# Kernel optimization log

Measured on AMD Instinct MI355X. Metric: run time of the kernel, lower is better.

## Reference

```python
import jax, jax.numpy as jnp
import numpy as np

N = 50000     # nodes
E = 800000    # edges (before self-loops)
DIN = 128     # input feature dim
DH = 16       # per-head hidden dim (layer 1)
H = 8         # heads (layer 1)
DOUT = 64     # output classes (layer 2, heads=1)


def setup_inputs() -> dict:
    key = jax.random.key(0)
    ks = jax.random.split(key, 10)
    def rn(k, shape, scale=0.1):
        return jax.random.normal(k, shape, dtype=jnp.float32) * scale
    x = jax.random.normal(ks[0], (N, DIN), dtype=jnp.float32)
    edge_index = jax.random.randint(ks[1], (2, E), 0, N, dtype=jnp.int64)
    return {
        "x": x,
        "edge_index": edge_index,
        "W1": rn(ks[2], (DIN, H * DH)),
        "a_src1": rn(ks[3], (H, DH)),
        "a_dst1": rn(ks[4], (H, DH)),
        "b1": jnp.zeros((H * DH,), jnp.float32),
        "W2": rn(ks[5], (H * DH, DOUT)),
        "a_src2": rn(ks[6], (1, DOUT)),
        "a_dst2": rn(ks[7], (1, DOUT)),
        "b2": jnp.zeros((DOUT,), jnp.float32),
    }


def gat_conv(x, src, dst, W, a_src, a_dst, b, heads, out_dim):
    """PyG-style GATConv: edge attention + segment softmax over dst + scatter-add."""
    n = x.shape[0]
    h = (x @ W).reshape(n, heads, out_dim)                 # [N, H, D]
    alpha_src = jnp.sum(h * a_src, axis=-1)                # [N, H]
    alpha_dst = jnp.sum(h * a_dst, axis=-1)                # [N, H]
    e = jax.nn.leaky_relu(alpha_src[src] + alpha_dst[dst], 0.2)  # [Etot, H]
    # numerically-stable segment softmax grouped by destination node
    m = jax.ops.segment_max(e, dst, num_segments=n)        # [N, H]
    ex = jnp.exp(e - m[dst])
    s = jax.ops.segment_sum(ex, dst, num_segments=n)       # [N, H]
    alpha = ex / (s[dst] + 1e-16)                          # [Etot, H]
    msg = h[src] * alpha[..., None]                        # [Etot, H, D]
    out = jax.ops.segment_sum(msg, dst, num_segments=n)    # [N, H, D]
    return out.reshape(n, heads * out_dim) + b


def reference(x, W1, a_src1, a_dst1, b1, W2, a_src2, a_dst2, b2, edge_index):
    # eval mode: F.dropout(p=0.6, training=False) is identity
    loop = jnp.arange(N, dtype=edge_index.dtype)
    src = jnp.concatenate([edge_index[0], loop])  # add_self_loops=True (PyG default)
    dst = jnp.concatenate([edge_index[1], loop])
    h = gat_conv(x, src, dst, W1, a_src1, a_dst1, b1, H, DH)
    h = jax.nn.elu(h)
    h = gat_conv(h, src, dst, W2, a_src2, a_dst2, b2, 1, DOUT)
    return (h, jax.nn.log_softmax(h, axis=1))
```

## Files before the change

kernel.cpp:

```cpp
#include <hip/hip_runtime.h>

#define NN 50000
#define EE 800000
#define ET (EE + NN)
#define NCH ((NN + 255) / 256)
#define DEGB ((ET + 255) / 256)
#define WPB ((128 * 128 + 128 * 64 + 255) / 256)
#define GEMB ((NN + 63) / 64)

typedef unsigned short ushort_t;
using bf16x8 = __attribute__((ext_vector_type(8))) short;
using f32x4  = __attribute__((ext_vector_type(4))) float;

__device__ __forceinline__ float bf2f(ushort_t u) {
    return __uint_as_float(((unsigned int)u) << 16);
}
__device__ __forceinline__ ushort_t f2bf(float f) {
    unsigned int u = __float_as_uint(f);
    u += 0x7fffu + ((u >> 16) & 1u);
    return (ushort_t)(u >> 16);
}
__device__ __forceinline__ float lrelu(float e) {
    return fmaxf(e, 0.f) + 0.2f * fminf(e, 0.f);
}
__device__ __forceinline__ float ldf(const void* p, int i, bool f32) {
    return f32 ? ((const float*)p)[i] : bf2f(((const ushort_t*)p)[i]);
}

__device__ __forceinline__ bool sniff_f32(const unsigned int* __restrict__ xw) {
    int lane = threadIdx.x & 63;
    float v = __uint_as_float(xw[lane]);
    float a = fabsf(v);
    bool ok = (a > 1e-6f && a < 1e6f) || v == 0.f;
    unsigned long long m = __ballot(ok);
    return __popcll(m) >= 48;
}
__device__ __forceinline__ bool sniff_i64(const int* __restrict__ eiw) {
    int lane = threadIdx.x & 63;
    unsigned long long m = __ballot(eiw[2 * lane + 1] != 0);
    return __popcll(m) <= 4;
}

__device__ __forceinline__ void edge_sd(const int* ei, int i, bool i64, int& s, int& d) {
    if (i < EE) {
        if (i64) { s = ei[2 * i]; d = ei[2 * (EE + i)]; }
        else     { s = ei[i];     d = ei[EE + i]; }
    } else {
        s = d = i - EE;
    }
}
__device__ __forceinline__ int edge_d(const int* ei, int i, bool i64) {
    if (i < EE) return i64 ? ei[2 * (EE + i)] : ei[EE + i];
    return i - EE;
}

__global__ __launch_bounds__(256) void prep_kernel(const int* __restrict__ ei, int* __restrict__ deg8,
                                                   const unsigned int* __restrict__ xw,
                                                   const void* W1v, const void* W2v,
                                                   ushort_t* __restrict__ Wt1, ushort_t* __restrict__ Wt2) {
    int b = blockIdx.x;
    if (b < DEGB) {
        bool i64 = sniff_i64(ei);
        int i = b * 256 + threadIdx.x;
        if (i >= ET) return;
        int g = b & 7;
        int d = edge_d(ei, i, i64);
        atomicAdd(&deg8[(size_t)g * NN + d], 1);
    } else {
        bool f32 = sniff_f32(xw);
        int i = (b - DEGB) * 256 + threadIdx.x;
        if (i < 128 * 128) {
            int k = i >> 7, nc = i & 127;
            ushort_t v = f32 ? f2bf(((const float*)W1v)[i]) : ((const ushort_t*)W1v)[i];
            Wt1[nc * 128 + k] = v;
        }
        int j = i - 128 * 128;
        if (j >= 0 && j < 128 * 64) {
            int k = j >> 6, nc = j & 63;
            ushort_t v = f32 ? f2bf(((const float*)W2v)[j]) : ((const ushort_t*)W2v)[j];
            Wt2[nc * 128 + k] = v;
        }
    }
}

#define FLG_A (1ull << 62)
#define FLG_P (2ull << 62)

__device__ void scan_body(int b, int* __restrict__ deg8, int* __restrict__ rowptr,
                          unsigned long long* __restrict__ state) {
    __shared__ int wsum[4];
    __shared__ int bpref;
    int t = threadIdx.x;
    int node = b * 256 + t;
    int lane = t & 63, wid = t >> 6;
    int dv[8];
    int v = 0;
    if (node < NN) {
        #pragma unroll
        for (int g = 0; g < 8; ++g) {
            dv[g] = deg8[(size_t)g * NN + node];
            v += dv[g];
        }
    }
    int x = v;
    #pragma unroll
    for (int off = 1; off < 64; off <<= 1) {
        int y = __shfl_up(x, off);
        if (lane >= off) x += y;
    }
    if (lane == 63) wsum[wid] = x;
    __syncthreads();
    if (t < 4) {
        int s = wsum[t];
        #pragma unroll
        for (int off = 1; off < 4; off <<= 1) {
            int y = __shfl_up(s, off);
            if (t >= off) s += y;
        }
        wsum[t] = s;
    }
    __syncthreads();
    int total = wsum[3];
    if (t == 0) {
        int prefix = 0;
        if (b == 0) {
            atomicExch(&state[0], FLG_P | (unsigned long long)(unsigned)total);
        } else {
            atomicExch(&state[b], FLG_A | (unsigned long long)(unsigned)total);
            int j = b - 1;
            while (true) {
                unsigned long long sv = atomicAdd(&state[j], 0ull);
                unsigned long long f = sv >> 62;
                if (f == 0) { __builtin_amdgcn_s_sleep(2); continue; }
                prefix += (int)(unsigned)(sv & 0xffffffffull);
                if (f == 2) break;
                --j;
            }
            atomicExch(&state[b], FLG_P | (unsigned long long)(unsigned)(prefix + total));
        }
        bpref = prefix;
    }
    __syncthreads();
    int excl = x - v + ((wid > 0) ? wsum[wid - 1] : 0);
    if (node < NN) {
        int run = bpref + excl;
        rowptr[node] = run;
        #pragma unroll
        for (int g = 0; g < 8; ++g) {
            deg8[(size_t)g * NN + node] = run;
            run += dv[g];
        }
    }
    if (b == NCH - 1 && t == 255) rowptr[NN] = bpref + total;
}

template <bool AEXT, int NCOL, int NH>
__device__ __forceinline__ void mgemm_body(int bid, const void* Av, const ushort_t* __restrict__ Wt,
                                           const void* a_src, const void* a_dst,
                                           ushort_t* __restrict__ outb, float* __restrict__ asrc,
                                           float* __restrict__ adst, int n, bool f32) {
    constexpr int K = 128;
    constexpr int NCT = NCOL / 16;
    bool af32 = AEXT && f32;
    int t = threadIdx.x;
    int lane = t & 63, wid = t >> 6;
    int m = lane & 15, quad = lane >> 4;
    int rbase = bid * 64 + wid * 16;
    int row = rbase + m;
    bool rok = row < n;

    bf16x8 af[4];
    if (rok) {
        if (!af32) {
            const ushort_t* ap = (const ushort_t*)Av + (size_t)row * K + quad * 8;
            #pragma unroll
            for (int kk = 0; kk < 4; ++kk) af[kk] = *(const bf16x8*)(ap + kk * 32);
        } else {
            const float* ap = (const float*)Av + (size_t)row * K + quad * 8;
            #pragma unroll
            for (int kk = 0; kk < 4; ++kk) {
                float4 q0 = *(const float4*)(ap + kk * 32);
                float4 q1 = *(const float4*)(ap + kk * 32 + 4);
                bf16x8 v;
                v[0] = (short)f2bf(q0.x); v[1] = (short)f2bf(q0.y);
                v[2] = (short)f2bf(q0.z); v[3] = (short)f2bf(q0.w);
                v[4] = (short)f2bf(q1.x); v[5] = (short)f2bf(q1.y);
                v[6] = (short)f2bf(q1.z); v[7] = (short)f2bf(q1.w);
                af[kk] = v;
            }
        }
    } else {
        #pragma unroll
        for (int kk = 0; kk < 4; ++kk) af[kk] = (bf16x8){0, 0, 0, 0, 0, 0, 0, 0};
    }

    f32x4 acc[NCT];
    #pragma unroll
    for (int c = 0; c < NCT; ++c) acc[c] = (f32x4){0.f, 0.f, 0.f, 0.f};

    const ushort_t* wp = Wt + (size_t)m * K + quad * 8;
    #pragma unroll
    for (int c = 0; c < NCT; ++c) {
        const ushort_t* wc = wp + (size_t)c * 16 * K;
        #pragma unroll
        for (int kk = 0; kk < 4; ++kk) {
            bf16x8 bf = *(const bf16x8*)(wc + kk * 32);
            acc[c] = __builtin_amdgcn_mfma_f32_16x16x32_bf16(af[kk], bf, acc[c], 0, 0, 0);
        }
    }

    int orow0 = rbase + quad * 4;
    #pragma unroll
    for (int c = 0; c < NCT; ++c) {
        #pragma unroll
        for (int r = 0; r < 4; ++r) {
            int orow = orow0 + r;
            if (orow < n) outb[(size_t)orow * NCOL + c * 16 + m] = f2bf(acc[c][r]);
        }
    }

    if (NH == 8) {
        #pragma unroll
        for (int c = 0; c < NCT; ++c) {
            float as = ldf(a_src, c * 16 + m, f32);
            float ad = ldf(a_dst, c * 16 + m, f32);
            float ps[4], pd[4];
            #pragma unroll
            for (int r = 0; r < 4; ++r) { ps[r] = acc[c][r] * as; pd[r] = acc[c][r] * ad; }
            #pragma unroll
            for (int stp = 1; stp < 16; stp <<= 1) {
                #pragma unroll
                for (int r = 0; r < 4; ++r) {
                    ps[r] += __shfl_xor(ps[r], stp);
                    pd[r] += __shfl_xor(pd[r], stp);
                }
            }
            if (m == 0) {
                #pragma unroll
                for (int r = 0; r < 4; ++r) {
                    int orow = orow0 + r;
                    if (orow < n) {
                        asrc[(size_t)orow * 8 + c] = ps[r];
                        adst[(size_t)orow * 8 + c] = pd[r];
                    }
                }
            }
        }
    } else {
        float ps[4] = {0.f, 0.f, 0.f, 0.f}, pd[4] = {0.f, 0.f, 0.f, 0.f};
        #pragma unroll
        for (int c = 0; c < NCT; ++c) {
            float as = ldf(a_src, c * 16 + m, f32);
            float ad = ldf(a_dst, c * 16 + m, f32);
            #pragma unroll
            for (int r = 0; r < 4; ++r) {
                ps[r] = fmaf(acc[c][r], as, ps[r]);
                pd[r] = fmaf(acc[c][r], ad, pd[r]);
            }
        }
        #pragma unroll
        for (int stp = 1; stp < 16; stp <<= 1) {
            #pragma unroll
            for (int r = 0; r < 4; ++r) {
                ps[r] += __shfl_xor(ps[r], stp);
                pd[r] += __shfl_xor(pd[r], stp);
            }
        }
        if (m == 0) {
            #pragma unroll
            for (int r = 0; r < 4; ++r) {
                int orow = orow0 + r;
                if (orow < n) { asrc[orow] = ps[r]; adst[orow] = pd[r]; }
            }
        }
    }
}

__global__ __launch_bounds__(256) void scan_mgemm1_kernel(int* __restrict__ deg8, int* __restrict__ rowptr,
                                                          unsigned long long* __restrict__ state,
                                                          const void* xv, const ushort_t* __restrict__ Wt1,
                                                          const void* as1, const void* ad1,
                                                          ushort_t* __restrict__ h1b,
                                                          float* __restrict__ asrc1, float* __restrict__ adst1) {
    if (blockIdx.x < NCH) {
        scan_body(blockIdx.x, deg8, rowptr, state);
        return;
    }
    bool f32 = sniff_f32((const unsigned int*)xv);
    mgemm_body<true, 128, 8>(blockIdx.x - NCH, xv, Wt1, as1, ad1, h1b, asrc1, adst1, NN, f32);
}

__global__ __launch_bounds__(256) void mgemm2_kernel(const void* Av, const ushort_t* __restrict__ Wt,
                                                     const void* a_src, const void* a_dst,
                                                     ushort_t* __restrict__ outb, float* __restrict__ asrc,
                                                     float* __restrict__ adst, const unsigned int* __restrict__ xw) {
    bool f32 = sniff_f32(xw);
    mgemm_body<false, 64, 1>(blockIdx.x, Av, Wt, a_src, a_dst, outb, asrc, adst, NN, f32);
}

__global__ __launch_bounds__(256) void fill_kernel(const int* __restrict__ ei, int* __restrict__ deg8,
                                                   int* __restrict__ col) {
    bool i64 = sniff_i64(ei);
    int i = blockIdx.x * 256 + threadIdx.x;
    if (i >= ET) return;
    int g = blockIdx.x & 7;
    int s, d;
    edge_sd(ei, i, i64, s, d);
    int pos = atomicAdd(&deg8[(size_t)g * NN + d], 1);
    col[pos] = s;
}

__global__ __launch_bounds__(256) void agg1_kernel(const unsigned int* __restrict__ xw,
                                                   const int* __restrict__ rowptr, const int* __restrict__ col,
                                                   const ushort_t* __restrict__ h1b,
                                                   const float* __restrict__ asrc, const float* __restrict__ adst,
                                                   const void* b1, ushort_t* __restrict__ hmidb) {
    __shared__ float wle[4][8 * 72];
    __shared__ int loff[4][64];
    bool f32 = sniff_f32(xw);
    int lane = threadIdx.x & 63, wid = threadIdx.x >> 6;
    int d = blockIdx.x * 4 + wid;
    if (d >= NN) return;
    int start = rowptr[d], end = rowptr[d + 1];
    int hB = lane >> 3;
    const float4* dp = (const float4*)(adst + (size_t)d * 8);
    float4 ad0 = dp[0], ad1 = dp[1];
    const char* hb = (const char*)h1b + lane * 4;
    float acc0 = 0.f, acc1 = 0.f, ssum = 0.f;
    for (int chunk = start; chunk < end; chunk += 64) {
        int cnt = min(64, end - chunk);
        int c = (chunk + lane < end) ? col[chunk + lane] : 0;
        loff[wid][lane] = c << 8;
        if (lane < cnt) {
            const float4* ap = (const float4*)(asrc + (size_t)c * 8);
            float4 s0 = ap[0], s1 = ap[1];
            wle[wid][0 * 72 + lane] = __expf(lrelu(s0.x + ad0.x));
            wle[wid][1 * 72 + lane] = __expf(lrelu(s0.y + ad0.y));
            wle[wid][2 * 72 + lane] = __expf(lrelu(s0.z + ad0.z));
            wle[wid][3 * 72 + lane] = __expf(lrelu(s0.w + ad0.w));
            wle[wid][4 * 72 + lane] = __expf(lrelu(s1.x + ad1.x));
            wle[wid][5 * 72 + lane] = __expf(lrelu(s1.y + ad1.y));
            wle[wid][6 * 72 + lane] = __expf(lrelu(s1.z + ad1.z));
            wle[wid][7 * 72 + lane] = __expf(lrelu(s1.w + ad1.w));
        }
        #pragma unroll 4
        for (int j = 0; j < cnt; ++j) {
            int off = loff[wid][j];
            float ex = wle[wid][hB * 72 + j];
            unsigned int hv = *(const unsigned int*)(hb + off);
            ssum += ex;
            acc0 = fmaf(ex, __uint_as_float(hv << 16), acc0);
            acc1 = fmaf(ex, __uint_as_float(hv & 0xffff0000u), acc1);
        }
    }
    float inv = 1.f / (ssum + 1e-16f);
    float o0 = fmaf(acc0, inv, ldf(b1, lane * 2, f32));
    float o1 = fmaf(acc1, inv, ldf(b1, lane * 2 + 1, f32));
    o0 = (o0 > 0.f) ? o0 : (__expf(o0) - 1.f);
    o1 = (o1 > 0.f) ? o1 : (__expf(o1) - 1.f);
    unsigned int pk = ((unsigned int)f2bf(o1) << 16) | (unsigned int)f2bf(o0);
    *(unsigned int*)(hmidb + (size_t)d * 128 + lane * 2) = pk;
}

__global__ __launch_bounds__(256) void agg2_kernel(const unsigned int* __restrict__ xw,
                                                   const int* __restrict__ rowptr, const int* __restrict__ col,
                                                   const ushort_t* __restrict__ h2b,
                                                   const float* __restrict__ asrc, const float* __restrict__ adst,
                                                   const void* b2, float* __restrict__ out) {
    __shared__ float wle[4][64];
    __shared__ int loff[4][64];
    bool f32 = sniff_f32(xw);
    int lane = threadIdx.x & 63, wid = threadIdx.x >> 6;
    int d = blockIdx.x * 4 + wid;
    if (d >= NN) return;
    int start = rowptr[d], end = rowptr[d + 1];
    float ad = adst[d];
    const char* hb = (const char*)h2b + lane * 2;
    float acc = 0.f, ssum = 0.f;
    for (int chunk = start; chunk < end; chunk += 64) {
        int cnt = min(64, end - chunk);
        int c = (chunk + lane < end) ? col[chunk + lane] : 0;
        loff[wid][lane] = c << 7;
        if (lane < cnt) wle[wid][lane] = __expf(lrelu(asrc[c] + ad));
        #pragma unroll 4
        for (int j = 0; j < cnt; ++j) {
            int off = loff[wid][j];
            float ex = wle[wid][j];
            float hv = bf2f(*(const ushort_t*)(hb + off));
            ssum += ex;
            acc = fmaf(ex, hv, acc);
        }
    }
    float o = acc / (ssum + 1e-16f) + ldf(b2, lane, f32);
    float mm = o;
    #pragma unroll
    for (int off = 1; off < 64; off <<= 1) mm = fmaxf(mm, __shfl_xor(mm, off));
    float texp = __expf(o - mm);
    float ts = texp;
    #pragma unroll
    for (int off = 1; off < 64; off <<= 1) ts += __shfl_xor(ts, off);
    float ls = o - mm - __logf(ts);
    out[(size_t)d * 64 + lane] = o;
    out[(size_t)NN * 64 + (size_t)d * 64 + lane] = ls;
}

extern "C" void kernel_launch(void* const* d_in, const int* in_sizes, int n_in,
                              void* d_out, int out_size, void* d_ws, size_t ws_size,
                              hipStream_t stream) {
    const void* x   = d_in[0];
    const int*  ei  = (const int*)d_in[1];
    const void* W1  = d_in[2];
    const void* as1 = d_in[3];
    const void* ad1 = d_in[4];
    const void* b1  = d_in[5];
    const void* W2  = d_in[6];
    const void* as2 = d_in[7];
    const void* ad2 = d_in[8];
    const void* b2  = d_in[9];
    float* out = (float*)d_out;

    char* w = (char*)d_ws;
    auto alloc = [&](size_t bytes) {
        void* p = (void*)w;
        w += (bytes + 255) & ~(size_t)255;
        return p;
    };
    int* deg8     = (int*)alloc((size_t)8 * NN * 4 + 4096);
    unsigned long long* state = (unsigned long long*)((char*)deg8 + (size_t)8 * NN * 4);
    int* rowptr   = (int*)alloc((size_t)(NN + 1) * 4);
    int* colx     = (int*)alloc((size_t)ET * 4);
    ushort_t* Wt1 = (ushort_t*)alloc((size_t)128 * 128 * 2);
    ushort_t* Wt2 = (ushort_t*)alloc((size_t)64 * 128 * 2);
    ushort_t* h1b = (ushort_t*)alloc((size_t)NN * 128 * 2);
    float* asrc1  = (float*)alloc((size_t)NN * 8 * 4);
    float* adst1  = (float*)alloc((size_t)NN * 8 * 4);
    ushort_t* hmidb = (ushort_t*)alloc((size_t)NN * 128 * 2);
    ushort_t* h2b = (ushort_t*)alloc((size_t)NN * 64 * 2);
    float* asrc2  = (float*)alloc((size_t)NN * 4);
    float* adst2  = (float*)alloc((size_t)NN * 4);

    hipMemsetAsync(deg8, 0, (size_t)8 * NN * 4 + (size_t)NCH * 8, stream);

    prep_kernel<<<DEGB + WPB, 256, 0, stream>>>(ei, deg8, (const unsigned int*)x, W1, W2, Wt1, Wt2);
    scan_mgemm1_kernel<<<NCH + GEMB, 256, 0, stream>>>(deg8, rowptr, state, x, Wt1, as1, ad1,
                                                       h1b, asrc1, adst1);
    fill_kernel<<<DEGB, 256, 0, stream>>>(ei, deg8, colx);
    agg1_kernel<<<(NN + 3) / 4, 256, 0, stream>>>((const unsigned int*)x, rowptr, colx, h1b,
                                                  asrc1, adst1, b1, hmidb);
    mgemm2_kernel<<<GEMB, 256, 0, stream>>>((const void*)hmidb, Wt2, as2, ad2, h2b, asrc2, adst2,
                                            (const unsigned int*)x);
    agg2_kernel<<<(NN + 3) / 4, 256, 0, stream>>>((const unsigned int*)x, rowptr, colx, h2b,
                                                  asrc2, adst2, b2, out);
}
```

Baseline: 291.6 us.

## Record edge ranks in degree count, atomic-free CSR fill fused with GEMM1

Result: faster. 253.4 us (-13.1%).

```diff
diff --git a/kernel.cpp b/kernel.cpp
--- a/kernel.cpp
+++ b/kernel.cpp
@@ -55,6 +55,7 @@
 }
 
 __global__ __launch_bounds__(256) void prep_kernel(const int* __restrict__ ei, int* __restrict__ deg8,
+                                                   int* __restrict__ rank,
                                                    const unsigned int* __restrict__ xw,
                                                    const void* W1v, const void* W2v,
                                                    ushort_t* __restrict__ Wt1, ushort_t* __restrict__ Wt2) {
@@ -65,7 +66,7 @@
         if (i >= ET) return;
         int g = b & 7;
         int d = edge_d(ei, i, i64);
-        atomicAdd(&deg8[(size_t)g * NN + d], 1);
+        rank[i] = atomicAdd(&deg8[(size_t)g * NN + d], 1);
     } else {
         bool f32 = sniff_f32(xw);
         int i = (b - DEGB) * 256 + threadIdx.x;
@@ -84,12 +85,12 @@
 }
 
 #define FLG_A (1ull << 62)
-#define FLG_P (2ull << 62)
-
-__device__ void scan_body(int b, int* __restrict__ deg8, int* __restrict__ rowptr,
-                          unsigned long long* __restrict__ state) {
+
+__global__ __launch_bounds__(256) void scan_kernel(int* __restrict__ deg8, int* __restrict__ rowptr,
+                                                   unsigned long long* __restrict__ state) {
     __shared__ int wsum[4];
     __shared__ int bpref;
+    int b = blockIdx.x;
     int t = threadIdx.x;
     int node = b * 256 + t;
     int lane = t & 63, wid = t >> 6;
@@ -121,24 +122,21 @@
     }
     __syncthreads();
     int total = wsum[3];
-    if (t == 0) {
-        int prefix = 0;
-        if (b == 0) {
-            atomicExch(&state[0], FLG_P | (unsigned long long)(unsigned)total);
-        } else {
-            atomicExch(&state[b], FLG_A | (unsigned long long)(unsigned)total);
-            int j = b - 1;
-            while (true) {
-                unsigned long long sv = atomicAdd(&state[j], 0ull);
-                unsigned long long f = sv >> 62;
-                if (f == 0) { __builtin_amdgcn_s_sleep(2); continue; }
-                prefix += (int)(unsigned)(sv & 0xffffffffull);
-                if (f == 2) break;
-                --j;
-            }
-            atomicExch(&state[b], FLG_P | (unsigned long long)(unsigned)(prefix + total));
-        }
-        bpref = prefix;
+    if (t == 0) atomicExch(&state[b], FLG_A | (unsigned long long)(unsigned)total);
+    if (t < 64) {
+        int p = 0;
+        #pragma unroll
+        for (int w = 0; w < (NCH + 63) / 64; ++w) {
+            int j = w * 64 + t;
+            unsigned long long sv = 0;
+            if (j < b) {
+                do { sv = atomicAdd(&state[j], 0ull); __builtin_amdgcn_s_sleep(1); } while (!(sv >> 62));
+            }
+            p += (int)(unsigned)(sv & 0xffffffffull);
+        }
+        #pragma unroll
+        for (int off = 1; off < 64; off <<= 1) p += __shfl_xor(p, off);
+        if (t == 0) bpref = p;
     }
     __syncthreads();
     int excl = x - v + ((wid > 0) ? wsum[wid - 1] : 0);
@@ -151,7 +149,7 @@
             run += dv[g];
         }
     }
-    if (b == NCH - 1 && t == 255) rowptr[NN] = bpref + total;
+    if (b == NCH - 1 && t == 0) rowptr[NN] = bpref + total;
 }
 
 template <bool AEXT, int NCOL, int NH>
@@ -276,18 +274,26 @@
     }
 }
 
-__global__ __launch_bounds__(256) void scan_mgemm1_kernel(int* __restrict__ deg8, int* __restrict__ rowptr,
-                                                          unsigned long long* __restrict__ state,
-                                                          const void* xv, const ushort_t* __restrict__ Wt1,
-                                                          const void* as1, const void* ad1,
-                                                          ushort_t* __restrict__ h1b,
-                                                          float* __restrict__ asrc1, float* __restrict__ adst1) {
-    if (blockIdx.x < NCH) {
-        scan_body(blockIdx.x, deg8, rowptr, state);
+__global__ __launch_bounds__(256) void gemm1_fill_kernel(const void* xv, const ushort_t* __restrict__ Wt1,
+                                                         const void* as1, const void* ad1,
+                                                         ushort_t* __restrict__ h1b,
+                                                         float* __restrict__ asrc1, float* __restrict__ adst1,
+                                                         const int* __restrict__ ei,
+                                                         const int* __restrict__ deg8off,
+                                                         const int* __restrict__ rank, int* __restrict__ col) {
+    if (blockIdx.x < GEMB) {
+        bool f32 = sniff_f32((const unsigned int*)xv);
+        mgemm_body<true, 128, 8>(blockIdx.x, xv, Wt1, as1, ad1, h1b, asrc1, adst1, NN, f32);
         return;
     }
-    bool f32 = sniff_f32((const unsigned int*)xv);
-    mgemm_body<true, 128, 8>(blockIdx.x - NCH, xv, Wt1, as1, ad1, h1b, asrc1, adst1, NN, f32);
+    int bb = blockIdx.x - GEMB;
+    bool i64 = sniff_i64(ei);
+    int i = bb * 256 + threadIdx.x;
+    if (i >= ET) return;
+    int g = bb & 7;
+    int s, d;
+    edge_sd(ei, i, i64, s, d);
+    col[deg8off[(size_t)g * NN + d] + rank[i]] = s;
 }
 
 __global__ __launch_bounds__(256) void mgemm2_kernel(const void* Av, const ushort_t* __restrict__ Wt,
@@ -296,18 +302,6 @@
                                                      float* __restrict__ adst, const unsigned int* __restrict__ xw) {
     bool f32 = sniff_f32(xw);
     mgemm_body<false, 64, 1>(blockIdx.x, Av, Wt, a_src, a_dst, outb, asrc, adst, NN, f32);
-}
-
-__global__ __launch_bounds__(256) void fill_kernel(const int* __restrict__ ei, int* __restrict__ deg8,
-                                                   int* __restrict__ col) {
-    bool i64 = sniff_i64(ei);
-    int i = blockIdx.x * 256 + threadIdx.x;
-    if (i >= ET) return;
-    int g = blockIdx.x & 7;
-    int s, d;
-    edge_sd(ei, i, i64, s, d);
-    int pos = atomicAdd(&deg8[(size_t)g * NN + d], 1);
-    col[pos] = s;
 }
 
 __global__ __launch_bounds__(256) void agg1_kernel(const unsigned int* __restrict__ xw,
@@ -343,7 +337,7 @@
             wle[wid][6 * 72 + lane] = __expf(lrelu(s1.z + ad1.z));
             wle[wid][7 * 72 + lane] = __expf(lrelu(s1.w + ad1.w));
         }
-        #pragma unroll 4
+        #pragma unroll 8
         for (int j = 0; j < cnt; ++j) {
             int off = loff[wid][j];
             float ex = wle[wid][hB * 72 + j];
@@ -382,7 +376,7 @@
         int c = (chunk + lane < end) ? col[chunk + lane] : 0;
         loff[wid][lane] = c << 7;
         if (lane < cnt) wle[wid][lane] = __expf(lrelu(asrc[c] + ad));
-        #pragma unroll 4
+        #pragma unroll 8
         for (int j = 0; j < cnt; ++j) {
             int off = loff[wid][j];
             float ex = wle[wid][j];
@@ -428,6 +422,7 @@
     int* deg8     = (int*)alloc((size_t)8 * NN * 4 + 4096);
     unsigned long long* state = (unsigned long long*)((char*)deg8 + (size_t)8 * NN * 4);
     int* rowptr   = (int*)alloc((size_t)(NN + 1) * 4);
+    int* rank     = (int*)alloc((size_t)ET * 4);
     int* colx     = (int*)alloc((size_t)ET * 4);
     ushort_t* Wt1 = (ushort_t*)alloc((size_t)128 * 128 * 2);
     ushort_t* Wt2 = (ushort_t*)alloc((size_t)64 * 128 * 2);
@@ -441,10 +436,10 @@
 
     hipMemsetAsync(deg8, 0, (size_t)8 * NN * 4 + (size_t)NCH * 8, stream);
 
-    prep_kernel<<<DEGB + WPB, 256, 0, stream>>>(ei, deg8, (const unsigned int*)x, W1, W2, Wt1, Wt2);
-    scan_mgemm1_kernel<<<NCH + GEMB, 256, 0, stream>>>(deg8, rowptr, state, x, Wt1, as1, ad1,
-                                                       h1b, asrc1, adst1);
-    fill_kernel<<<DEGB, 256, 0, stream>>>(ei, deg8, colx);
+    prep_kernel<<<DEGB + WPB, 256, 0, stream>>>(ei, deg8, rank, (const unsigned int*)x, W1, W2, Wt1, Wt2);
+    scan_kernel<<<NCH, 256, 0, stream>>>(deg8, rowptr, state);
+    gemm1_fill_kernel<<<GEMB + DEGB, 256, 0, stream>>>(x, Wt1, as1, ad1, h1b, asrc1, adst1,
+                                                       ei, deg8, rank, colx);
     agg1_kernel<<<(NN + 3) / 4, 256, 0, stream>>>((const unsigned int*)x, rowptr, colx, h1b,
                                                   asrc1, adst1, b1, hmidb);
     mgemm2_kernel<<<GEMB, 256, 0, stream>>>((const void*)hmidb, Wt2, as2, ad2, h2b, asrc2, adst2,
```
